# Performance work log

Hardware: AMD Instinct MI355X
Metric: run time of the kernel (lower is better)

Reference implementation:

```python
import jax, jax.numpy as jnp
import numpy as np

N = 40000          # nodes
E = 640000         # directed edges (before self-loops)
NEG_SLOPE = 0.2    # PyG GATConv default negative_slope


def _segment_softmax(e, dst, n):
    # e: [E, H] per-edge logits, softmax over edges sharing the same dst
    m = jax.ops.segment_max(e, dst, num_segments=n)          # [n, H]
    ex = jnp.exp(e - m[dst])
    s = jax.ops.segment_sum(ex, dst, num_segments=n)         # [n, H]
    return ex / (s[dst] + 1e-16)


def _gat_layer(x, src, dst, W, att_src, att_dst, bias, heads, out_ch, concat, n):
    h = (x @ W).reshape(n, heads, out_ch)                    # [n, H, C]
    a_s = jnp.einsum('nhc,hc->nh', h, att_src)               # [n, H]
    a_d = jnp.einsum('nhc,hc->nh', h, att_dst)
    e = jax.nn.leaky_relu(a_s[src] + a_d[dst], NEG_SLOPE)    # [E, H]
    alpha = _segment_softmax(e, dst, n)                      # [E, H]
    msg = h[src] * alpha[:, :, None]                         # [E, H, C]
    out = jax.ops.segment_sum(msg, dst, num_segments=n)      # [n, H, C]
    out = out.reshape(n, heads * out_ch) if concat else out.mean(axis=1)
    return out + bias


def setup_inputs():
    key = jax.random.key(0)
    ks = jax.random.split(key, 12)
    x = jax.random.normal(ks[0], (N, 128), dtype=jnp.float32)
    edge_index = jax.random.randint(ks[1], (2, E), 0, N, dtype=jnp.int64)
    weights = jax.random.uniform(ks[2], (E,), dtype=jnp.float32)
    # GATConv(128, 64, heads=2)
    W1 = jax.random.normal(ks[3], (128, 2 * 64), dtype=jnp.float32) * 0.1
    att_src1 = jax.random.normal(ks[4], (2, 64), dtype=jnp.float32) * 0.1
    att_dst1 = jax.random.normal(ks[5], (2, 64), dtype=jnp.float32) * 0.1
    b1 = jnp.zeros((128,), dtype=jnp.float32)
    # GATConv(128, 4, heads=1, concat=False)
    W2 = jax.random.normal(ks[6], (128, 4), dtype=jnp.float32) * 0.1
    att_src2 = jax.random.normal(ks[7], (1, 4), dtype=jnp.float32) * 0.1
    att_dst2 = jax.random.normal(ks[8], (1, 4), dtype=jnp.float32) * 0.1
    b2 = jnp.zeros((4,), dtype=jnp.float32)
    return {'x': x, 'edge_index': edge_index, 'weights': weights,
            'W1': W1, 'att_src1': att_src1, 'att_dst1': att_dst1, 'b1': b1,
            'W2': W2, 'att_src2': att_src2, 'att_dst2': att_dst2, 'b2': b2}


def reference(x, edge_index, weights, W1, att_src1, att_dst1, b1, W2, att_src2, att_dst2, b2):
    # PyG default add_self_loops=True
    loop = jnp.arange(N, dtype=edge_index.dtype)
    src = jnp.concatenate([edge_index[0], loop])
    dst = jnp.concatenate([edge_index[1], loop])
    # dropout layers are identity in eval mode; `weights` unused (as in source)
    h = _gat_layer(x, src, dst, W1, att_src1, att_dst1, b1, 2, 64, True, N)
    h = jax.nn.elu(h)
    h = _gat_layer(h, src, dst, W2, att_src2, att_dst2, b2, 1, 4, False, N)
    return jax.nn.softmax(h, axis=1)
```

## Files before the change

### kernel.cpp

```cpp
#include <hip/hip_runtime.h>
#include <hip/hip_bf16.h>
#include <math.h>

#define N_NODES 40000
#define N_EDGES 640000
#define ET (N_EDGES + N_NODES)
#define SCAN_BLOCKS 40
#define SCAN_CHUNK 1000

__device__ __forceinline__ float wave_red_sum(float v) {
#pragma unroll
  for (int m = 32; m >= 1; m >>= 1) v += __shfl_xor(v, m, 64);
  return v;
}
__device__ __forceinline__ int wave_red_sum_i(int v) {
#pragma unroll
  for (int m = 32; m >= 1; m >>= 1) v += __shfl_xor(v, m, 64);
  return v;
}
__device__ __forceinline__ float half_red_sum(float v) {
#pragma unroll
  for (int m = 16; m >= 1; m >>= 1) v += __shfl_xor(v, m, 64);
  return v;
}

__global__ void k_hist(const int* __restrict__ ei, int* __restrict__ deg,
                       int* __restrict__ erank) {
  int i = blockIdx.x * blockDim.x + threadIdx.x;
  if (i >= ET) return;
  int d = (i < N_EDGES) ? ei[N_EDGES + i] : (i - N_EDGES);
  erank[i] = atomicAdd(&deg[d], 1);
}

__global__ __launch_bounds__(1024) void k_scanA(const int* __restrict__ deg,
                                                int* __restrict__ blocksum) {
  int t = threadIdx.x;
  int idx = blockIdx.x * SCAN_CHUNK + t;
  int v = (t < SCAN_CHUNK) ? deg[idx] : 0;
  int lane = t & 63, w = t >> 6;
  int s = wave_red_sum_i(v);
  __shared__ int ws[16];
  if (lane == 0) ws[w] = s;
  __syncthreads();
  if (t == 0) {
    int r = 0;
#pragma unroll
    for (int k = 0; k < 16; k++) r += ws[k];
    blocksum[blockIdx.x] = r;
  }
}

__global__ __launch_bounds__(1024) void k_scanB(const int* __restrict__ deg,
                                                const int* __restrict__ blocksum,
                                                int* __restrict__ off) {
  int t = threadIdx.x;
  int b = blockIdx.x;
  int lane = t & 63, w = t >> 6;
  __shared__ int carry_s;
  __shared__ int ws[16];
  if (w == 0) {
    int bs = (lane < b) ? blocksum[lane] : 0;
    int c = wave_red_sum_i(bs);
    if (lane == 0) carry_s = c;
  }
  int idx = b * SCAN_CHUNK + t;
  int v = (t < SCAN_CHUNK) ? deg[idx] : 0;
  int p = v;
#pragma unroll
  for (int o = 1; o < 64; o <<= 1) {
    int u = __shfl_up(p, o, 64);
    if (lane >= o) p += u;
  }
  if (lane == 63) ws[w] = p;
  __syncthreads();
  if (t == 0) {
    int r = 0;
#pragma unroll
    for (int k = 0; k < 16; k++) { int x = ws[k]; ws[k] = r; r += x; }
  }
  __syncthreads();
  int excl = carry_s + ws[w] + p - v;
  if (t < SCAN_CHUNK) off[idx] = excl;
  if (b == SCAN_BLOCKS - 1 && t == SCAN_CHUNK - 1) off[N_NODES] = excl + v;
}

__global__ void k_fill(const int* __restrict__ ei, const int* __restrict__ off,
                       const int* __restrict__ erank, int* __restrict__ csr_src) {
  int i = blockIdx.x * blockDim.x + threadIdx.x;
  if (i >= ET) return;
  int s, d;
  if (i < N_EDGES) { s = ei[i]; d = ei[N_EDGES + i]; }
  else             { s = d = i - N_EDGES; }
  csr_src[off[d] + erank[i]] = s;
}

__global__ __launch_bounds__(256) void k_gemm1(
    const float* __restrict__ x, const float* __restrict__ W1,
    const float* __restrict__ asv, const float* __restrict__ adv,
    __hip_bfloat16* __restrict__ h1b, float* __restrict__ a_s, float* __restrict__ a_d) {
  __shared__ float xs[32 * 128];
  int t = threadIdx.x;
  int n0 = blockIdx.x * 32;
  {
    const float4* xg = (const float4*)(x + (size_t)n0 * 128);
    float4* xs4 = (float4*)xs;
#pragma unroll
    for (int i = 0; i < 4; i++) xs4[t + i * 256] = xg[t + i * 256];
  }
  __syncthreads();

  int lane = t & 63;
  int g = t >> 6;
  int c0 = lane * 2;
  const float4* xs4 = (const float4*)(xs + (size_t)g * 8 * 128);

  float2 acc[8];
#pragma unroll
  for (int j = 0; j < 8; j++) acc[j] = make_float2(0.f, 0.f);

  float2 w0 = *(const float2*)(W1 + (size_t)0 * 128 + c0);
  float2 w1 = *(const float2*)(W1 + (size_t)1 * 128 + c0);
  float2 w2 = *(const float2*)(W1 + (size_t)2 * 128 + c0);
  float2 w3 = *(const float2*)(W1 + (size_t)3 * 128 + c0);

  for (int k4 = 0; k4 < 32; k4++) {
    float2 nw0, nw1, nw2, nw3;
    if (k4 < 31) {
      nw0 = *(const float2*)(W1 + (size_t)(4 * k4 + 4) * 128 + c0);
      nw1 = *(const float2*)(W1 + (size_t)(4 * k4 + 5) * 128 + c0);
      nw2 = *(const float2*)(W1 + (size_t)(4 * k4 + 6) * 128 + c0);
      nw3 = *(const float2*)(W1 + (size_t)(4 * k4 + 7) * 128 + c0);
    }
#pragma unroll
    for (int j = 0; j < 8; j++) {
      float4 xv = xs4[j * 32 + k4];
      acc[j].x = fmaf(xv.x, w0.x, acc[j].x);
      acc[j].y = fmaf(xv.x, w0.y, acc[j].y);
      acc[j].x = fmaf(xv.y, w1.x, acc[j].x);
      acc[j].y = fmaf(xv.y, w1.y, acc[j].y);
      acc[j].x = fmaf(xv.z, w2.x, acc[j].x);
      acc[j].y = fmaf(xv.z, w2.y, acc[j].y);
      acc[j].x = fmaf(xv.w, w3.x, acc[j].x);
      acc[j].y = fmaf(xv.w, w3.y, acc[j].y);
    }
    w0 = nw0; w1 = nw1; w2 = nw2; w3 = nw3;
  }

  float2 av_s = *(const float2*)(asv + c0);
  float2 av_d = *(const float2*)(adv + c0);
  int head = lane >> 5;
#pragma unroll
  for (int j = 0; j < 8; j++) {
    int n = n0 + g * 8 + j;
    __hip_bfloat162 hv;
    hv.x = __float2bfloat16(acc[j].x);
    hv.y = __float2bfloat16(acc[j].y);
    *(__hip_bfloat162*)(h1b + (size_t)n * 128 + c0) = hv;
    float rs = half_red_sum(acc[j].x * av_s.x + acc[j].y * av_s.y);
    float rd = half_red_sum(acc[j].x * av_d.x + acc[j].y * av_d.y);
    if ((lane & 31) == 0) {
      a_s[n * 2 + head] = rs;
      a_d[n * 2 + head] = rd;
    }
  }
}

__global__ __launch_bounds__(256) void k_agg1(
    const int* __restrict__ off, const int* __restrict__ csr_src,
    const float* __restrict__ a_s, const float* __restrict__ a_d,
    const __hip_bfloat16* __restrict__ h1b, const float* __restrict__ b1,
    const float* __restrict__ W2, const float* __restrict__ as2,
    const float* __restrict__ ad2,
    float* __restrict__ h2, float* __restrict__ a_s2, float* __restrict__ a_d2) {
  int v = blockIdx.x * 4 + (threadIdx.x >> 6);
  int lane = threadIdx.x & 63;
  int head = lane >> 5;
  int beg = off[v], end = off[v + 1];
  float2 Ad = *(const float2*)(a_d + 2 * v);
  const __hip_bfloat162* h1b2 = (const __hip_bfloat162*)h1b;

  float acc0 = 0.f, acc1 = 0.f;
  float sum0 = 0.f, sum1 = 0.f;
  for (int base = beg; base < end; base += 64) {
    int idx = base + lane;
    int sreg = 0;
    float ex0 = 0.f, ex1 = 0.f;
    if (idx < end) {
      sreg = csr_src[idx];
      float2 As = *(const float2*)(a_s + 2 * sreg);
      float e0 = As.x + Ad.x; e0 = (e0 >= 0.f) ? e0 : 0.2f * e0;
      float e1 = As.y + Ad.y; e1 = (e1 >= 0.f) ? e1 : 0.2f * e1;
      ex0 = __expf(e0); ex1 = __expf(e1);
    }
    sum0 += ex0; sum1 += ex1;
    int jmax = min(64, end - base);
    int j = 0;
    for (; j + 4 <= jmax; j += 4) {
      int sA = __shfl(sreg, j + 0, 64);
      int sB = __shfl(sreg, j + 1, 64);
      int sC = __shfl(sreg, j + 2, 64);
      int sD = __shfl(sreg, j + 3, 64);
      float xA0 = __shfl(ex0, j + 0, 64), xA1 = __shfl(ex1, j + 0, 64);
      float xB0 = __shfl(ex0, j + 1, 64), xB1 = __shfl(ex1, j + 1, 64);
      float xC0 = __shfl(ex0, j + 2, 64), xC1 = __shfl(ex1, j + 2, 64);
      float xD0 = __shfl(ex0, j + 3, 64), xD1 = __shfl(ex1, j + 3, 64);
      __hip_bfloat162 hA = h1b2[(size_t)sA * 64 + lane];
      __hip_bfloat162 hB = h1b2[(size_t)sB * 64 + lane];
      __hip_bfloat162 hC = h1b2[(size_t)sC * 64 + lane];
      __hip_bfloat162 hD = h1b2[(size_t)sD * 64 + lane];
      float eA = head ? xA1 : xA0;
      float eB = head ? xB1 : xB0;
      float eC = head ? xC1 : xC0;
      float eD = head ? xD1 : xD0;
      acc0 = fmaf(eA, __bfloat162float(hA.x), acc0);
      acc1 = fmaf(eA, __bfloat162float(hA.y), acc1);
      acc0 = fmaf(eB, __bfloat162float(hB.x), acc0);
      acc1 = fmaf(eB, __bfloat162float(hB.y), acc1);
      acc0 = fmaf(eC, __bfloat162float(hC.x), acc0);
      acc1 = fmaf(eC, __bfloat162float(hC.y), acc1);
      acc0 = fmaf(eD, __bfloat162float(hD.x), acc0);
      acc1 = fmaf(eD, __bfloat162float(hD.y), acc1);
    }
    for (; j < jmax; j++) {
      int s = __shfl(sreg, j, 64);
      float x0 = __shfl(ex0, j, 64);
      float x1 = __shfl(ex1, j, 64);
      float ex = head ? x1 : x0;
      __hip_bfloat162 hv = h1b2[(size_t)s * 64 + lane];
      acc0 = fmaf(ex, __bfloat162float(hv.x), acc0);
      acc1 = fmaf(ex, __bfloat162float(hv.y), acc1);
    }
  }
  sum0 = wave_red_sum(sum0);
  sum1 = wave_red_sum(sum1);
  float inv = 1.f / ((head ? sum1 : sum0) + 1e-16f);

  float2 bv = *(const float2*)(b1 + 2 * lane);
  float o0 = acc0 * inv + bv.x;
  float o1 = acc1 * inv + bv.y;
  o0 = (o0 > 0.f) ? o0 : expm1f(o0);
  o1 = (o1 > 0.f) ? o1 : expm1f(o1);

  float4 wA = *(const float4*)(W2 + (2 * lane) * 4);
  float4 wB = *(const float4*)(W2 + (2 * lane + 1) * 4);
  float p0 = wave_red_sum(o0 * wA.x + o1 * wB.x);
  float p1 = wave_red_sum(o0 * wA.y + o1 * wB.y);
  float p2 = wave_red_sum(o0 * wA.z + o1 * wB.z);
  float p3 = wave_red_sum(o0 * wA.w + o1 * wB.w);
  if (lane == 0) {
    float4 q = {p0, p1, p2, p3};
    *(float4*)(h2 + (size_t)v * 4) = q;
    a_s2[v] = p0 * as2[0] + p1 * as2[1] + p2 * as2[2] + p3 * as2[3];
    a_d2[v] = p0 * ad2[0] + p1 * ad2[1] + p2 * ad2[2] + p3 * ad2[3];
  }
}

__global__ __launch_bounds__(256) void k_agg2(
    const int* __restrict__ off, const int* __restrict__ csr_src,
    const float* __restrict__ a_s, const float* __restrict__ a_d,
    const float* __restrict__ h2, const float* __restrict__ b2,
    float* __restrict__ out) {
  int v = blockIdx.x * 4 + (threadIdx.x >> 6);
  int lane = threadIdx.x & 63;
  int beg = off[v], end = off[v + 1];
  float adv = a_d[v];

  float sum = 0.f;
  float4 acc = {0.f, 0.f, 0.f, 0.f};
  for (int i = beg + lane; i < end; i += 64) {
    int s = csr_src[i];
    float e = a_s[s] + adv;
    e = (e >= 0.f) ? e : 0.2f * e;
    float ex = __expf(e);
    sum += ex;
    float4 hv = *(const float4*)(h2 + (size_t)s * 4);
    acc.x = fmaf(ex, hv.x, acc.x);
    acc.y = fmaf(ex, hv.y, acc.y);
    acc.z = fmaf(ex, hv.z, acc.z);
    acc.w = fmaf(ex, hv.w, acc.w);
  }
  sum = wave_red_sum(sum);
  acc.x = wave_red_sum(acc.x);
  acc.y = wave_red_sum(acc.y);
  acc.z = wave_red_sum(acc.z);
  acc.w = wave_red_sum(acc.w);

  if (lane == 0) {
    float invd = 1.f / (sum + 1e-16f);
    float o0 = acc.x * invd + b2[0];
    float o1 = acc.y * invd + b2[1];
    float o2 = acc.z * invd + b2[2];
    float o3 = acc.w * invd + b2[3];
    float mx = fmaxf(fmaxf(o0, o1), fmaxf(o2, o3));
    float e0 = __expf(o0 - mx), e1 = __expf(o1 - mx);
    float e2 = __expf(o2 - mx), e3 = __expf(o3 - mx);
    float s4 = e0 + e1 + e2 + e3;
    float4 r = {e0 / s4, e1 / s4, e2 / s4, e3 / s4};
    *(float4*)(out + (size_t)v * 4) = r;
  }
}

extern "C" void kernel_launch(void* const* d_in, const int* in_sizes, int n_in,
                              void* d_out, int out_size, void* d_ws, size_t ws_size,
                              hipStream_t stream) {
  const float* x   = (const float*)d_in[0];
  const int*   ei  = (const int*)d_in[1];
  const float* W1  = (const float*)d_in[3];
  const float* as1 = (const float*)d_in[4];
  const float* ad1 = (const float*)d_in[5];
  const float* b1  = (const float*)d_in[6];
  const float* W2  = (const float*)d_in[7];
  const float* as2 = (const float*)d_in[8];
  const float* ad2 = (const float*)d_in[9];
  const float* b2  = (const float*)d_in[10];
  float* out = (float*)d_out;

  char* w = (char*)d_ws;
  auto alloc = [&](size_t bytes) {
    char* p = w;
    w += (bytes + 255) & ~(size_t)255;
    return p;
  };
  int*   deg     = (int*)alloc((size_t)N_NODES * 4);
  int*   off     = (int*)alloc((size_t)(N_NODES + 1) * 4);
  int*   erank   = (int*)alloc((size_t)ET * 4);
  int*   csr_src = (int*)alloc((size_t)ET * 4);
  int*   blocksum= (int*)alloc((size_t)SCAN_BLOCKS * 4);
  __hip_bfloat16* h1b = (__hip_bfloat16*)alloc((size_t)N_NODES * 128 * 2);
  float* a_s1w   = (float*)alloc((size_t)N_NODES * 2 * 4);
  float* a_d1w   = (float*)alloc((size_t)N_NODES * 2 * 4);
  float* h2      = (float*)alloc((size_t)N_NODES * 4 * 4);
  float* a_s2w   = (float*)alloc((size_t)N_NODES * 4);
  float* a_d2w   = (float*)alloc((size_t)N_NODES * 4);

  hipMemsetAsync(deg, 0, (size_t)N_NODES * 4, stream);
  k_hist<<<(ET + 255) / 256, 256, 0, stream>>>(ei, deg, erank);
  k_scanA<<<SCAN_BLOCKS, 1024, 0, stream>>>(deg, blocksum);
  k_scanB<<<SCAN_BLOCKS, 1024, 0, stream>>>(deg, blocksum, off);
  k_fill<<<(ET + 255) / 256, 256, 0, stream>>>(ei, off, erank, csr_src);

  k_gemm1<<<N_NODES / 32, 256, 0, stream>>>(x, W1, as1, ad1, h1b, a_s1w, a_d1w);
  k_agg1<<<N_NODES / 4, 256, 0, stream>>>(off, csr_src, a_s1w, a_d1w, h1b, b1,
                                          W2, as2, ad2, h2, a_s2w, a_d2w);
  k_agg2<<<N_NODES / 4, 256, 0, stream>>>(off, csr_src, a_s2w, a_d2w, h2, b2, out);
}
```

Measured before the change: 211.4 us.

## Split layer-1 edge softmax weights into separate kernel and pack layer-2 node data

Adds a k_exp kernel that computes per-edge exp attention weights and per-node sums for layer 1 and writes them to a workspace array. k_agg1 then reads these weights and source indices with uniform (scalar) loads instead of the shuffle-based broadcast, with readfirstlane on the edge range. Layer-2 features and source attention logits are packed into one 32-byte record per node, so each gathered edge in k_agg2 reads one contiguous record. The cost is an extra launch and an extra round trip of about 5.4MB of edge weights through memory.

```diff
diff --git a/kernel.cpp b/kernel.cpp
--- a/kernel.cpp
+++ b/kernel.cpp
@@ -165,75 +165,81 @@
   }
 }
 
+__global__ __launch_bounds__(256) void k_exp(
+    const int* __restrict__ off, const int* __restrict__ csr_src,
+    const float* __restrict__ a_s, const float* __restrict__ a_d,
+    float2* __restrict__ exw, float* __restrict__ sums) {
+  int v = blockIdx.x * 4 + (threadIdx.x >> 6);
+  int lane = threadIdx.x & 63;
+  int beg = off[v], end = off[v + 1];
+  float2 Ad = *(const float2*)(a_d + 2 * v);
+  float s0 = 0.f, s1 = 0.f;
+  for (int i = beg + lane; i < end; i += 64) {
+    int s = csr_src[i];
+    float2 As = *(const float2*)(a_s + 2 * s);
+    float e0 = As.x + Ad.x; e0 = (e0 >= 0.f) ? e0 : 0.2f * e0;
+    float e1 = As.y + Ad.y; e1 = (e1 >= 0.f) ? e1 : 0.2f * e1;
+    float x0 = __expf(e0), x1 = __expf(e1);
+    exw[i] = make_float2(x0, x1);
+    s0 += x0; s1 += x1;
+  }
+  s0 = wave_red_sum(s0);
+  s1 = wave_red_sum(s1);
+  if (lane == 0) { sums[2 * v] = s0; sums[2 * v + 1] = s1; }
+}
+
 __global__ __launch_bounds__(256) void k_agg1(
     const int* __restrict__ off, const int* __restrict__ csr_src,
-    const float* __restrict__ a_s, const float* __restrict__ a_d,
+    const float2* __restrict__ exw, const float* __restrict__ sums,
     const __hip_bfloat16* __restrict__ h1b, const float* __restrict__ b1,
     const float* __restrict__ W2, const float* __restrict__ as2,
     const float* __restrict__ ad2,
-    float* __restrict__ h2, float* __restrict__ a_s2, float* __restrict__ a_d2) {
+    float* __restrict__ h2pack, float* __restrict__ a_d2) {
   int v = blockIdx.x * 4 + (threadIdx.x >> 6);
   int lane = threadIdx.x & 63;
   int head = lane >> 5;
-  int beg = off[v], end = off[v + 1];
-  float2 Ad = *(const float2*)(a_d + 2 * v);
+  int beg = __builtin_amdgcn_readfirstlane(off[v]);
+  int end = __builtin_amdgcn_readfirstlane(off[v + 1]);
+  float2 sv = *(const float2*)(sums + 2 * v);
+  float inv = 1.f / ((head ? sv.y : sv.x) + 1e-16f);
   const __hip_bfloat162* h1b2 = (const __hip_bfloat162*)h1b;
 
   float acc0 = 0.f, acc1 = 0.f;
-  float sum0 = 0.f, sum1 = 0.f;
-  for (int base = beg; base < end; base += 64) {
-    int idx = base + lane;
-    int sreg = 0;
-    float ex0 = 0.f, ex1 = 0.f;
-    if (idx < end) {
-      sreg = csr_src[idx];
-      float2 As = *(const float2*)(a_s + 2 * sreg);
-      float e0 = As.x + Ad.x; e0 = (e0 >= 0.f) ? e0 : 0.2f * e0;
-      float e1 = As.y + Ad.y; e1 = (e1 >= 0.f) ? e1 : 0.2f * e1;
-      ex0 = __expf(e0); ex1 = __expf(e1);
-    }
-    sum0 += ex0; sum1 += ex1;
-    int jmax = min(64, end - base);
-    int j = 0;
-    for (; j + 4 <= jmax; j += 4) {
-      int sA = __shfl(sreg, j + 0, 64);
-      int sB = __shfl(sreg, j + 1, 64);
-      int sC = __shfl(sreg, j + 2, 64);
-      int sD = __shfl(sreg, j + 3, 64);
-      float xA0 = __shfl(ex0, j + 0, 64), xA1 = __shfl(ex1, j + 0, 64);
-      float xB0 = __shfl(ex0, j + 1, 64), xB1 = __shfl(ex1, j + 1, 64);
-      float xC0 = __shfl(ex0, j + 2, 64), xC1 = __shfl(ex1, j + 2, 64);
-      float xD0 = __shfl(ex0, j + 3, 64), xD1 = __shfl(ex1, j + 3, 64);
-      __hip_bfloat162 hA = h1b2[(size_t)sA * 64 + lane];
-      __hip_bfloat162 hB = h1b2[(size_t)sB * 64 + lane];
-      __hip_bfloat162 hC = h1b2[(size_t)sC * 64 + lane];
-      __hip_bfloat162 hD = h1b2[(size_t)sD * 64 + lane];
-      float eA = head ? xA1 : xA0;
-      float eB = head ? xB1 : xB0;
-      float eC = head ? xC1 : xC0;
-      float eD = head ? xD1 : xD0;
-      acc0 = fmaf(eA, __bfloat162float(hA.x), acc0);
-      acc1 = fmaf(eA, __bfloat162float(hA.y), acc1);
-      acc0 = fmaf(eB, __bfloat162float(hB.x), acc0);
-      acc1 = fmaf(eB, __bfloat162float(hB.y), acc1);
-      acc0 = fmaf(eC, __bfloat162float(hC.x), acc0);
-      acc1 = fmaf(eC, __bfloat162float(hC.y), acc1);
-      acc0 = fmaf(eD, __bfloat162float(hD.x), acc0);
-      acc1 = fmaf(eD, __bfloat162float(hD.y), acc1);
-    }
-    for (; j < jmax; j++) {
-      int s = __shfl(sreg, j, 64);
-      float x0 = __shfl(ex0, j, 64);
-      float x1 = __shfl(ex1, j, 64);
-      float ex = head ? x1 : x0;
-      __hip_bfloat162 hv = h1b2[(size_t)s * 64 + lane];
-      acc0 = fmaf(ex, __bfloat162float(hv.x), acc0);
-      acc1 = fmaf(ex, __bfloat162float(hv.y), acc1);
-    }
-  }
-  sum0 = wave_red_sum(sum0);
-  sum1 = wave_red_sum(sum1);
-  float inv = 1.f / ((head ? sum1 : sum0) + 1e-16f);
+  int i = beg;
+  for (; i + 4 <= end; i += 4) {
+    int sA = csr_src[i + 0];
+    int sB = csr_src[i + 1];
+    int sC = csr_src[i + 2];
+    int sD = csr_src[i + 3];
+    float2 wA = exw[i + 0];
+    float2 wB = exw[i + 1];
+    float2 wC = exw[i + 2];
+    float2 wD = exw[i + 3];
+    __hip_bfloat162 hA = h1b2[(size_t)sA * 64 + lane];
+    __hip_bfloat162 hB = h1b2[(size_t)sB * 64 + lane];
+    __hip_bfloat162 hC = h1b2[(size_t)sC * 64 + lane];
+    __hip_bfloat162 hD = h1b2[(size_t)sD * 64 + lane];
+    float eA = head ? wA.y : wA.x;
+    float eB = head ? wB.y : wB.x;
+    float eC = head ? wC.y : wC.x;
+    float eD = head ? wD.y : wD.x;
+    acc0 = fmaf(eA, __bfloat162float(hA.x), acc0);
+    acc1 = fmaf(eA, __bfloat162float(hA.y), acc1);
+    acc0 = fmaf(eB, __bfloat162float(hB.x), acc0);
+    acc1 = fmaf(eB, __bfloat162float(hB.y), acc1);
+    acc0 = fmaf(eC, __bfloat162float(hC.x), acc0);
+    acc1 = fmaf(eC, __bfloat162float(hC.y), acc1);
+    acc0 = fmaf(eD, __bfloat162float(hD.x), acc0);
+    acc1 = fmaf(eD, __bfloat162float(hD.y), acc1);
+  }
+  for (; i < end; i++) {
+    int s = csr_src[i];
+    float2 wv = exw[i];
+    float ex = head ? wv.y : wv.x;
+    __hip_bfloat162 hv = h1b2[(size_t)s * 64 + lane];
+    acc0 = fmaf(ex, __bfloat162float(hv.x), acc0);
+    acc1 = fmaf(ex, __bfloat162float(hv.y), acc1);
+  }
 
   float2 bv = *(const float2*)(b1 + 2 * lane);
   float o0 = acc0 * inv + bv.x;
@@ -249,35 +255,37 @@
   float p3 = wave_red_sum(o0 * wA.w + o1 * wB.w);
   if (lane == 0) {
     float4 q = {p0, p1, p2, p3};
-    *(float4*)(h2 + (size_t)v * 4) = q;
-    a_s2[v] = p0 * as2[0] + p1 * as2[1] + p2 * as2[2] + p3 * as2[3];
+    *(float4*)(h2pack + (size_t)v * 8) = q;
+    h2pack[(size_t)v * 8 + 4] =
+        p0 * as2[0] + p1 * as2[1] + p2 * as2[2] + p3 * as2[3];
     a_d2[v] = p0 * ad2[0] + p1 * ad2[1] + p2 * ad2[2] + p3 * ad2[3];
   }
 }
 
 __global__ __launch_bounds__(256) void k_agg2(
     const int* __restrict__ off, const int* __restrict__ csr_src,
-    const float* __restrict__ a_s, const float* __restrict__ a_d,
-    const float* __restrict__ h2, const float* __restrict__ b2,
-    float* __restrict__ out) {
+    const float* __restrict__ h2pack, const float* __restrict__ a_d,
+    const float* __restrict__ b2, float* __restrict__ out) {
   int v = blockIdx.x * 4 + (threadIdx.x >> 6);
   int lane = threadIdx.x & 63;
   int beg = off[v], end = off[v + 1];
   float adv = a_d[v];
+  const float4* pk = (const float4*)h2pack;
 
   float sum = 0.f;
   float4 acc = {0.f, 0.f, 0.f, 0.f};
   for (int i = beg + lane; i < end; i += 64) {
     int s = csr_src[i];
-    float e = a_s[s] + adv;
+    float4 r0 = pk[2 * s];
+    float4 r1 = pk[2 * s + 1];
+    float e = r1.x + adv;
     e = (e >= 0.f) ? e : 0.2f * e;
     float ex = __expf(e);
     sum += ex;
-    float4 hv = *(const float4*)(h2 + (size_t)s * 4);
-    acc.x = fmaf(ex, hv.x, acc.x);
-    acc.y = fmaf(ex, hv.y, acc.y);
-    acc.z = fmaf(ex, hv.z, acc.z);
-    acc.w = fmaf(ex, hv.w, acc.w);
+    acc.x = fmaf(ex, r0.x, acc.x);
+    acc.y = fmaf(ex, r0.y, acc.y);
+    acc.z = fmaf(ex, r0.z, acc.z);
+    acc.w = fmaf(ex, r0.w, acc.w);
   }
   sum = wave_red_sum(sum);
   acc.x = wave_red_sum(acc.x);
@@ -329,8 +337,9 @@
   __hip_bfloat16* h1b = (__hip_bfloat16*)alloc((size_t)N_NODES * 128 * 2);
   float* a_s1w   = (float*)alloc((size_t)N_NODES * 2 * 4);
   float* a_d1w   = (float*)alloc((size_t)N_NODES * 2 * 4);
-  float* h2      = (float*)alloc((size_t)N_NODES * 4 * 4);
-  float* a_s2w   = (float*)alloc((size_t)N_NODES * 4);
+  float2* exw    = (float2*)alloc((size_t)ET * 8);
+  float* sums    = (float*)alloc((size_t)N_NODES * 2 * 4);
+  float* h2pack  = (float*)alloc((size_t)N_NODES * 8 * 4);
   float* a_d2w   = (float*)alloc((size_t)N_NODES * 4);
 
   hipMemsetAsync(deg, 0, (size_t)N_NODES * 4, stream);
@@ -340,7 +349,8 @@
   k_fill<<<(ET + 255) / 256, 256, 0, stream>>>(ei, off, erank, csr_src);
 
   k_gemm1<<<N_NODES / 32, 256, 0, stream>>>(x, W1, as1, ad1, h1b, a_s1w, a_d1w);
-  k_agg1<<<N_NODES / 4, 256, 0, stream>>>(off, csr_src, a_s1w, a_d1w, h1b, b1,
-                                          W2, as2, ad2, h2, a_s2w, a_d2w);
-  k_agg2<<<N_NODES / 4, 256, 0, stream>>>(off, csr_src, a_s2w, a_d2w, h2, b2, out);
-}
+  k_exp<<<N_NODES / 4, 256, 0, stream>>>(off, csr_src, a_s1w, a_d1w, exw, sums);
+  k_agg1<<<N_NODES / 4, 256, 0, stream>>>(off, csr_src, exw, sums, h1b, b1,
+                                          W2, as2, ad2, h2pack, a_d2w);
+  k_agg2<<<N_NODES / 4, 256, 0, stream>>>(off, csr_src, h2pack, a_d2w, b2, out);
+}
```

Measured after the change: 212.3 us. Within noise of the previous version (+0.4%).

## Fuse degree histogram into layer-1 GEMM, stage edges in LDS, pack layer-2 node data

Applied to the files above, without the earlier changes.

Merges the destination-degree histogram (atomic rank assignment) into the first-layer GEMM kernel: each of the 1250 blocks also processes 544 edges while its x tile loads are in flight. This removes one launch and overlaps the atomics with the x load. In the layer-1 aggregation, the per-wave broadcast of source ids and exp weights now goes through LDS instead of repeated shuffles. Layer-2 node features and the source attention score are packed into one 32-byte record so each edge needs one contiguous gather. The LDS staging relies on only a block-scope fence rather than a barrier, so it depends on wavefront lockstep for correctness.

```diff
diff --git a/kernel.cpp b/kernel.cpp
--- a/kernel.cpp
+++ b/kernel.cpp
@@ -7,6 +7,8 @@
 #define ET (N_EDGES + N_NODES)
 #define SCAN_BLOCKS 40
 #define SCAN_CHUNK 1000
+#define G1_BLOCKS 1250
+#define EPB 544
 
 __device__ __forceinline__ float wave_red_sum(float v) {
 #pragma unroll
@@ -22,14 +24,6 @@
 #pragma unroll
   for (int m = 16; m >= 1; m >>= 1) v += __shfl_xor(v, m, 64);
   return v;
-}
-
-__global__ void k_hist(const int* __restrict__ ei, int* __restrict__ deg,
-                       int* __restrict__ erank) {
-  int i = blockIdx.x * blockDim.x + threadIdx.x;
-  if (i >= ET) return;
-  int d = (i < N_EDGES) ? ei[N_EDGES + i] : (i - N_EDGES);
-  erank[i] = atomicAdd(&deg[d], 1);
 }
 
 __global__ __launch_bounds__(1024) void k_scanA(const int* __restrict__ deg,
@@ -97,16 +91,38 @@
 __global__ __launch_bounds__(256) void k_gemm1(
     const float* __restrict__ x, const float* __restrict__ W1,
     const float* __restrict__ asv, const float* __restrict__ adv,
+    const int* __restrict__ ei, int* __restrict__ deg, int* __restrict__ erank,
     __hip_bfloat16* __restrict__ h1b, float* __restrict__ a_s, float* __restrict__ a_d) {
   __shared__ float xs[32 * 128];
   int t = threadIdx.x;
   int n0 = blockIdx.x * 32;
+
+  const float4* xg = (const float4*)(x + (size_t)n0 * 128);
+  float4 xr0 = xg[t + 0 * 256];
+  float4 xr1 = xg[t + 1 * 256];
+  float4 xr2 = xg[t + 2 * 256];
+  float4 xr3 = xg[t + 3 * 256];
+
   {
-    const float4* xg = (const float4*)(x + (size_t)n0 * 128);
-    float4* xs4 = (float4*)xs;
-#pragma unroll
-    for (int i = 0; i < 4; i++) xs4[t + i * 256] = xg[t + i * 256];
-  }
+    int ebase = blockIdx.x * EPB;
+#pragma unroll
+    for (int r = 0; r < 2; r++) {
+      int i = ebase + r * 256 + t;
+      int d = (i < N_EDGES) ? ei[N_EDGES + i] : (i - N_EDGES);
+      erank[i] = atomicAdd(&deg[d], 1);
+    }
+    if (t < EPB - 512) {
+      int i = ebase + 512 + t;
+      int d = (i < N_EDGES) ? ei[N_EDGES + i] : (i - N_EDGES);
+      erank[i] = atomicAdd(&deg[d], 1);
+    }
+  }
+
+  float4* xs4w = (float4*)xs;
+  xs4w[t + 0 * 256] = xr0;
+  xs4w[t + 1 * 256] = xr1;
+  xs4w[t + 2 * 256] = xr2;
+  xs4w[t + 3 * 256] = xr3;
   __syncthreads();
 
   int lane = t & 63;
@@ -171,13 +187,17 @@
     const __hip_bfloat16* __restrict__ h1b, const float* __restrict__ b1,
     const float* __restrict__ W2, const float* __restrict__ as2,
     const float* __restrict__ ad2,
-    float* __restrict__ h2, float* __restrict__ a_s2, float* __restrict__ a_d2) {
-  int v = blockIdx.x * 4 + (threadIdx.x >> 6);
+    float* __restrict__ h2pack, float* __restrict__ a_d2) {
+  int wv = threadIdx.x >> 6;
+  int v = blockIdx.x * 4 + wv;
   int lane = threadIdx.x & 63;
   int head = lane >> 5;
   int beg = off[v], end = off[v + 1];
   float2 Ad = *(const float2*)(a_d + 2 * v);
   const __hip_bfloat162* h1b2 = (const __hip_bfloat162*)h1b;
+
+  __shared__ int    lds_s[4][64];
+  __shared__ float2 lds_e[4][64];
 
   float acc0 = 0.f, acc1 = 0.f;
   float sum0 = 0.f, sum1 = 0.f;
@@ -193,25 +213,29 @@
       ex0 = __expf(e0); ex1 = __expf(e1);
     }
     sum0 += ex0; sum1 += ex1;
+    lds_s[wv][lane] = sreg;
+    lds_e[wv][lane] = make_float2(ex0, ex1);
+    __threadfence_block();
+
     int jmax = min(64, end - base);
     int j = 0;
     for (; j + 4 <= jmax; j += 4) {
-      int sA = __shfl(sreg, j + 0, 64);
-      int sB = __shfl(sreg, j + 1, 64);
-      int sC = __shfl(sreg, j + 2, 64);
-      int sD = __shfl(sreg, j + 3, 64);
-      float xA0 = __shfl(ex0, j + 0, 64), xA1 = __shfl(ex1, j + 0, 64);
-      float xB0 = __shfl(ex0, j + 1, 64), xB1 = __shfl(ex1, j + 1, 64);
-      float xC0 = __shfl(ex0, j + 2, 64), xC1 = __shfl(ex1, j + 2, 64);
-      float xD0 = __shfl(ex0, j + 3, 64), xD1 = __shfl(ex1, j + 3, 64);
+      int sA = lds_s[wv][j + 0];
+      int sB = lds_s[wv][j + 1];
+      int sC = lds_s[wv][j + 2];
+      int sD = lds_s[wv][j + 3];
+      float2 wA = lds_e[wv][j + 0];
+      float2 wB = lds_e[wv][j + 1];
+      float2 wC = lds_e[wv][j + 2];
+      float2 wD = lds_e[wv][j + 3];
       __hip_bfloat162 hA = h1b2[(size_t)sA * 64 + lane];
       __hip_bfloat162 hB = h1b2[(size_t)sB * 64 + lane];
       __hip_bfloat162 hC = h1b2[(size_t)sC * 64 + lane];
       __hip_bfloat162 hD = h1b2[(size_t)sD * 64 + lane];
-      float eA = head ? xA1 : xA0;
-      float eB = head ? xB1 : xB0;
-      float eC = head ? xC1 : xC0;
-      float eD = head ? xD1 : xD0;
+      float eA = head ? wA.y : wA.x;
+      float eB = head ? wB.y : wB.x;
+      float eC = head ? wC.y : wC.x;
+      float eD = head ? wD.y : wD.x;
       acc0 = fmaf(eA, __bfloat162float(hA.x), acc0);
       acc1 = fmaf(eA, __bfloat162float(hA.y), acc1);
       acc0 = fmaf(eB, __bfloat162float(hB.x), acc0);
@@ -222,14 +246,14 @@
       acc1 = fmaf(eD, __bfloat162float(hD.y), acc1);
     }
     for (; j < jmax; j++) {
-      int s = __shfl(sreg, j, 64);
-      float x0 = __shfl(ex0, j, 64);
-      float x1 = __shfl(ex1, j, 64);
-      float ex = head ? x1 : x0;
+      int s = lds_s[wv][j];
+      float2 wv2 = lds_e[wv][j];
+      float ex = head ? wv2.y : wv2.x;
       __hip_bfloat162 hv = h1b2[(size_t)s * 64 + lane];
       acc0 = fmaf(ex, __bfloat162float(hv.x), acc0);
       acc1 = fmaf(ex, __bfloat162float(hv.y), acc1);
     }
+    __threadfence_block();
   }
   sum0 = wave_red_sum(sum0);
   sum1 = wave_red_sum(sum1);
@@ -249,35 +273,37 @@
   float p3 = wave_red_sum(o0 * wA.w + o1 * wB.w);
   if (lane == 0) {
     float4 q = {p0, p1, p2, p3};
-    *(float4*)(h2 + (size_t)v * 4) = q;
-    a_s2[v] = p0 * as2[0] + p1 * as2[1] + p2 * as2[2] + p3 * as2[3];
+    *(float4*)(h2pack + (size_t)v * 8) = q;
+    h2pack[(size_t)v * 8 + 4] =
+        p0 * as2[0] + p1 * as2[1] + p2 * as2[2] + p3 * as2[3];
     a_d2[v] = p0 * ad2[0] + p1 * ad2[1] + p2 * ad2[2] + p3 * ad2[3];
   }
 }
 
 __global__ __launch_bounds__(256) void k_agg2(
     const int* __restrict__ off, const int* __restrict__ csr_src,
-    const float* __restrict__ a_s, const float* __restrict__ a_d,
-    const float* __restrict__ h2, const float* __restrict__ b2,
-    float* __restrict__ out) {
+    const float* __restrict__ h2pack, const float* __restrict__ a_d,
+    const float* __restrict__ b2, float* __restrict__ out) {
   int v = blockIdx.x * 4 + (threadIdx.x >> 6);
   int lane = threadIdx.x & 63;
   int beg = off[v], end = off[v + 1];
   float adv = a_d[v];
+  const float4* pk = (const float4*)h2pack;
 
   float sum = 0.f;
   float4 acc = {0.f, 0.f, 0.f, 0.f};
   for (int i = beg + lane; i < end; i += 64) {
     int s = csr_src[i];
-    float e = a_s[s] + adv;
+    float4 r0 = pk[2 * s];
+    float4 r1 = pk[2 * s + 1];
+    float e = r1.x + adv;
     e = (e >= 0.f) ? e : 0.2f * e;
     float ex = __expf(e);
     sum += ex;
-    float4 hv = *(const float4*)(h2 + (size_t)s * 4);
-    acc.x = fmaf(ex, hv.x, acc.x);
-    acc.y = fmaf(ex, hv.y, acc.y);
-    acc.z = fmaf(ex, hv.z, acc.z);
-    acc.w = fmaf(ex, hv.w, acc.w);
+    acc.x = fmaf(ex, r0.x, acc.x);
+    acc.y = fmaf(ex, r0.y, acc.y);
+    acc.z = fmaf(ex, r0.z, acc.z);
+    acc.w = fmaf(ex, r0.w, acc.w);
   }
   sum = wave_red_sum(sum);
   acc.x = wave_red_sum(acc.x);
@@ -329,18 +355,17 @@
   __hip_bfloat16* h1b = (__hip_bfloat16*)alloc((size_t)N_NODES * 128 * 2);
   float* a_s1w   = (float*)alloc((size_t)N_NODES * 2 * 4);
   float* a_d1w   = (float*)alloc((size_t)N_NODES * 2 * 4);
-  float* h2      = (float*)alloc((size_t)N_NODES * 4 * 4);
-  float* a_s2w   = (float*)alloc((size_t)N_NODES * 4);
+  float* h2pack  = (float*)alloc((size_t)N_NODES * 8 * 4);
   float* a_d2w   = (float*)alloc((size_t)N_NODES * 4);
 
   hipMemsetAsync(deg, 0, (size_t)N_NODES * 4, stream);
-  k_hist<<<(ET + 255) / 256, 256, 0, stream>>>(ei, deg, erank);
+  k_gemm1<<<G1_BLOCKS, 256, 0, stream>>>(x, W1, as1, ad1, ei, deg, erank,
+                                         h1b, a_s1w, a_d1w);
   k_scanA<<<SCAN_BLOCKS, 1024, 0, stream>>>(deg, blocksum);
   k_scanB<<<SCAN_BLOCKS, 1024, 0, stream>>>(deg, blocksum, off);
   k_fill<<<(ET + 255) / 256, 256, 0, stream>>>(ei, off, erank, csr_src);
 
-  k_gemm1<<<N_NODES / 32, 256, 0, stream>>>(x, W1, as1, ad1, h1b, a_s1w, a_d1w);
   k_agg1<<<N_NODES / 4, 256, 0, stream>>>(off, csr_src, a_s1w, a_d1w, h1b, b1,
-                                          W2, as2, ad2, h2, a_s2w, a_d2w);
-  k_agg2<<<N_NODES / 4, 256, 0, stream>>>(off, csr_src, a_s2w, a_d2w, h2, b2, out);
-}
+                                          W2, as2, ad2, h2pack, a_d2w);
+  k_agg2<<<N_NODES / 4, 256, 0, stream>>>(off, csr_src, h2pack, a_d2w, b2, out);
+}
```

After: 201.2 us. 4.8% less time.
